# Kernel tuning notes

Measured on AMD Instinct MI355X. Metric: run time of the kernel, lower is better.

## Reference

```python
import jax, jax.numpy as jnp
import numpy as np

N, IN_F, OUT_F, K = 256, 8192, 8320, 16
J = OUT_F - IN_F  # 128


def setup_inputs() -> dict:
    key = jax.random.key(0)
    k1, k2 = jax.random.split(key)
    tensor = jax.random.normal(k1, (N, IN_F), dtype=jnp.float32)
    T = jax.random.normal(k2, (IN_F, J, K), dtype=jnp.float32)
    return {"tensor": tensor, "T": T}


def reference(tensor, T):
    # flatten(start_dim=1) is identity for rank-2 input
    x = tensor.reshape(tensor.shape[0], -1)            # [N, IN_F]
    feats = jnp.einsum('ni,ijk->njk', x, T)            # [N, J, K]
    # pairwise L1 across batch: [N,1,J,K] - [N,J,K] -> [N,N,J,K]
    diff = jnp.abs(feats[:, None, :, :] - feats[None, :, :, :])
    l1 = jnp.sum(diff, axis=3)                         # [N, N, J]
    diversity = jnp.sum(jnp.exp(-l1), axis=1)          # [N, J]
    return jnp.concatenate((x, diversity), axis=1)     # [N, IN_F + J]
```

## Files before the change

### kernel.cpp

```cpp
#include <hip/hip_runtime.h>

typedef unsigned int  u32;
typedef unsigned short u16;

typedef __bf16 bf16x8 __attribute__((ext_vector_type(8)));
typedef float  floatx4 __attribute__((ext_vector_type(4)));

#define N_ROWS 256
#define IN_F   8192
#define OUT_F  8320
#define JDIM   128
#define KDIM   16
#define JK     2048

#define BM     256
#define BN     64
#define BK     64
#define WSTRIDE 72

typedef const __attribute__((address_space(1))) u32 gu32;
typedef __attribute__((address_space(3))) u32 su32;

__device__ __forceinline__ u16 f2bf(float f) {
    u32 u = __float_as_uint(f);
    return (u16)((u + 0x7fffu + ((u >> 16) & 1u)) >> 16);
}
__device__ __forceinline__ float bf2f(u16 h) { return __uint_as_float(((u32)h) << 16); }

__global__ __launch_bounds__(256) void prep_kernel(const float* __restrict__ X,
                                                   float* __restrict__ out,
                                                   u16* __restrict__ Xb)
{
    int t = blockIdx.x * 256 + threadIdx.x;
    float4 v = reinterpret_cast<const float4*>(X)[t];
    int row = t >> 11;
    int c4  = t & 2047;
    reinterpret_cast<float4*>(out + (size_t)row * OUT_F)[c4] = v;
    ushort4 b;
    b.x = f2bf(v.x); b.y = f2bf(v.y); b.z = f2bf(v.z); b.w = f2bf(v.w);
    reinterpret_cast<ushort4*>(Xb)[t] = b;
    if (t < 8192) {
        int r2 = t >> 5, j4 = t & 31;
        reinterpret_cast<float4*>(out + (size_t)r2 * OUT_F + IN_F)[j4] = make_float4(0.f, 0.f, 0.f, 0.f);
    }
}

__global__ __launch_bounds__(256) void gemm_kernel(const u16* __restrict__ Xb,
                                                   const float* __restrict__ W,
                                                   u16* __restrict__ slabs,
                                                   int kchunk)
{
    __shared__ u16 xs[BM * BK];
    __shared__ u16 wt[BN * WSTRIDE];

    const int tid  = threadIdx.x;
    const int lane = tid & 63;
    const int wave = tid >> 6;
    const int c0   = blockIdx.x * BN;
    const int s    = blockIdx.y;
    const int k0base = s * kchunk;

    floatx4 acc[4][4] = {};

    const int xrl = lane >> 3;
    const int xgc = (lane & 7) ^ xrl;
    const int wk  = (tid >> 4) << 2;
    const int wc  = (tid & 15) << 2;

    const float* wptr = W + (size_t)(k0base + wk) * JK + c0 + wc;

    float4 wreg[4];
    #pragma unroll
    for (int r = 0; r < 4; ++r)
        wreg[r] = *(const float4*)(wptr + (size_t)r * JK);

    const int iters = kchunk >> 6;
    for (int it = 0; it < iters; ++it) {
        const int k0 = k0base + it * BK;
        __syncthreads();

        #pragma unroll
        for (int g = 0; g < 8; ++g) {
            int rbase = wave * 64 + g * 8;
            const u16* gp = Xb + (size_t)(rbase + xrl) * IN_F + k0 + xgc * 8;
            u32* lp = (u32*)&xs[rbase * BK];
            __builtin_amdgcn_global_load_lds((gu32*)gp, (su32*)lp, 16, 0, 0);
        }

        {
            const float* wr = (const float*)wreg;
            #pragma unroll
            for (int i = 0; i < 4; ++i) {
                u32 lo = (u32)f2bf(wr[0 * 4 + i]) | ((u32)f2bf(wr[1 * 4 + i]) << 16);
                u32 hi = (u32)f2bf(wr[2 * 4 + i]) | ((u32)f2bf(wr[3 * 4 + i]) << 16);
                uint2 v; v.x = lo; v.y = hi;
                *(uint2*)&wt[(wc + i) * WSTRIDE + wk] = v;
            }
        }
        __syncthreads();

        if (it + 1 < iters) {
            const float* wn = wptr + (size_t)(it + 1) * BK * JK;
            #pragma unroll
            for (int r = 0; r < 4; ++r)
                wreg[r] = *(const float4*)(wn + (size_t)r * JK);
        }

        const int mrow = lane & 15;
        const int q    = lane >> 4;
        #pragma unroll
        for (int h = 0; h < 2; ++h) {
            bf16x8 a[4], b[4];
            #pragma unroll
            for (int rt = 0; rt < 4; ++rt) {
                int rl   = wave * 64 + rt * 16 + mrow;
                int slot = (h * 4 + q) ^ (rl & 7);
                a[rt] = *reinterpret_cast<const bf16x8*>(&xs[rl * BK + slot * 8]);
            }
            #pragma unroll
            for (int ct = 0; ct < 4; ++ct) {
                int col = ct * 16 + mrow;
                b[ct] = *reinterpret_cast<const bf16x8*>(&wt[col * WSTRIDE + (h * 4 + q) * 8]);
            }
            #pragma unroll
            for (int rt = 0; rt < 4; ++rt)
                #pragma unroll
                for (int ct = 0; ct < 4; ++ct)
                    acc[rt][ct] = __builtin_amdgcn_mfma_f32_16x16x32_bf16(a[rt], b[ct], acc[rt][ct], 0, 0, 0);
        }
    }

    const int qe = lane >> 4;
    const int cl = lane & 15;
    u16* sp = slabs + (size_t)s * N_ROWS * JK;
    #pragma unroll
    for (int rt = 0; rt < 4; ++rt)
        #pragma unroll
        for (int ct = 0; ct < 4; ++ct)
            #pragma unroll
            for (int r = 0; r < 4; ++r) {
                int row = wave * 64 + rt * 16 + qe * 4 + r;
                int col = c0 + ct * 16 + cl;
                sp[(size_t)row * JK + col] = f2bf(acc[rt][ct][r]);
            }
}

__global__ __launch_bounds__(256) void reduce_kernel(const u16* __restrict__ slabs,
                                                     float* __restrict__ feats, int S)
{
    int t = blockIdx.x * 256 + threadIdx.x;
    float acc[8] = {};
    for (int s = 0; s < S; ++s) {
        uint4 v = *(const uint4*)(slabs + (size_t)s * N_ROWS * JK + (size_t)t * 8);
        const u16* h = (const u16*)&v;
        #pragma unroll
        for (int e = 0; e < 8; ++e) acc[e] += bf2f(h[e]);
    }
    float4* fp = (float4*)(feats + (size_t)t * 8);
    fp[0] = make_float4(acc[0], acc[1], acc[2], acc[3]);
    fp[1] = make_float4(acc[4], acc[5], acc[6], acc[7]);
}

__global__ __launch_bounds__(256) void pairwise_kernel(const float* __restrict__ feats,
                                                       float* __restrict__ out)
{
    const int j = blockIdx.x;
    const int mq = blockIdx.y;
    const int n = threadIdx.x;

    __shared__ float F[N_ROWS * KDIM];
    const float* fr = feats + (size_t)n * JK + j * KDIM;
    float4 v0 = ((const float4*)fr)[0];
    float4 v1 = ((const float4*)fr)[1];
    float4 v2 = ((const float4*)fr)[2];
    float4 v3 = ((const float4*)fr)[3];
    float4* Fp = (float4*)&F[n * KDIM];
    Fp[0] = v0; Fp[1] = v1; Fp[2] = v2; Fp[3] = v3;
    __syncthreads();

    float f[16] = { v0.x, v0.y, v0.z, v0.w, v1.x, v1.y, v1.z, v1.w,
                    v2.x, v2.y, v2.z, v2.w, v3.x, v3.y, v3.z, v3.w };
    float accum = 0.f;
    const int m0 = mq * 64;
    for (int m = 0; m < 64; ++m) {
        const float* Fm = &F[(m0 + m) * KDIM];
        float l1 = 0.f;
        #pragma unroll
        for (int k = 0; k < 16; ++k) l1 += fabsf(f[k] - Fm[k]);
        accum += exp2f(-1.4426950408889634f * l1);
    }
    atomicAdd(&out[(size_t)n * OUT_F + IN_F + j], accum);
}

extern "C" void kernel_launch(void* const* d_in, const int* in_sizes, int n_in,
                              void* d_out, int out_size, void* d_ws, size_t ws_size,
                              hipStream_t stream)
{
    const float* X = (const float*)d_in[0];
    const float* T = (const float*)d_in[1];
    float* out = (float*)d_out;

    float* feats = (float*)d_ws;
    u16*   Xb    = (u16*)((char*)d_ws + (2u << 20));
    u16*   slabs = (u16*)((char*)d_ws + (6u << 20));

    int S = 16;
    if (ws_size < (6u << 20) + (size_t)16 * N_ROWS * JK * 2) S = 8;
    if (ws_size < (6u << 20) + (size_t)8  * N_ROWS * JK * 2) S = 4;
    int kchunk = IN_F / S;

    prep_kernel<<<2048, 256, 0, stream>>>(X, out, Xb);
    gemm_kernel<<<dim3(JK / BN, S), 256, 0, stream>>>(Xb, T, slabs, kchunk);
    reduce_kernel<<<256, 256, 0, stream>>>(slabs, feats, S);
    pairwise_kernel<<<dim3(JDIM, 4), 256, 0, stream>>>(feats, out);
}
```

Measured before the change: 142.0 us.

## Fuse split-K reduction into pairwise kernel with j-major slab layout

The separate reduce kernel and the fp32 feats buffer are removed. The GEMM now writes its bf16 partial slabs in a j-major layout ([j][row][k]), so each pairwise block can sum the S partial slices for its own j directly while loading features. This saves one kernel launch and a global round trip through feats. In exchange, each of the 4 mq blocks per j re-reads and re-reduces the same slabs, and the GEMM epilogue stores have a different access pattern.

New measurement: 135.5 us. 4.6% less time.

```diff
diff --git a/kernel.cpp b/kernel.cpp
--- a/kernel.cpp
+++ b/kernel.cpp
@@ -17,6 +17,9 @@
 #define BN     64
 #define BK     64
 #define WSTRIDE 72
+
+#define SLAB_U16   (N_ROWS * JK)
+#define JSLICE_U16 (N_ROWS * KDIM)
 
 typedef const __attribute__((address_space(1))) u32 gu32;
 typedef __attribute__((address_space(3))) u32 su32;
@@ -132,56 +135,67 @@
 
     const int qe = lane >> 4;
     const int cl = lane & 15;
-    u16* sp = slabs + (size_t)s * N_ROWS * JK;
+    u16* sp = slabs + (size_t)s * SLAB_U16;
     #pragma unroll
     for (int rt = 0; rt < 4; ++rt)
         #pragma unroll
-        for (int ct = 0; ct < 4; ++ct)
+        for (int ct = 0; ct < 4; ++ct) {
+            int j = (c0 >> 4) + ct;
             #pragma unroll
             for (int r = 0; r < 4; ++r) {
                 int row = wave * 64 + rt * 16 + qe * 4 + r;
-                int col = c0 + ct * 16 + cl;
-                sp[(size_t)row * JK + col] = f2bf(acc[rt][ct][r]);
-            }
-}
-
-__global__ __launch_bounds__(256) void reduce_kernel(const u16* __restrict__ slabs,
-                                                     float* __restrict__ feats, int S)
-{
-    int t = blockIdx.x * 256 + threadIdx.x;
-    float acc[8] = {};
-    for (int s = 0; s < S; ++s) {
-        uint4 v = *(const uint4*)(slabs + (size_t)s * N_ROWS * JK + (size_t)t * 8);
-        const u16* h = (const u16*)&v;
-        #pragma unroll
-        for (int e = 0; e < 8; ++e) acc[e] += bf2f(h[e]);
-    }
-    float4* fp = (float4*)(feats + (size_t)t * 8);
-    fp[0] = make_float4(acc[0], acc[1], acc[2], acc[3]);
-    fp[1] = make_float4(acc[4], acc[5], acc[6], acc[7]);
-}
-
-__global__ __launch_bounds__(256) void pairwise_kernel(const float* __restrict__ feats,
+                sp[(size_t)j * JSLICE_U16 + row * KDIM + cl] = f2bf(acc[rt][ct][r]);
+            }
+        }
+}
+
+template<int S>
+__global__ __launch_bounds__(256) void fused_rp_kernel(const u16* __restrict__ slabs,
                                                        float* __restrict__ out)
 {
-    const int j = blockIdx.x;
+    const int j  = blockIdx.x;
     const int mq = blockIdx.y;
-    const int n = threadIdx.x;
+    const int n  = threadIdx.x;
 
     __shared__ float F[N_ROWS * KDIM];
-    const float* fr = feats + (size_t)n * JK + j * KDIM;
-    float4 v0 = ((const float4*)fr)[0];
-    float4 v1 = ((const float4*)fr)[1];
-    float4 v2 = ((const float4*)fr)[2];
-    float4 v3 = ((const float4*)fr)[3];
+
+    const u16* base = slabs + (size_t)j * JSLICE_U16 + n * KDIM;
+
+    float f[16];
+    #pragma unroll
+    for (int k = 0; k < 16; ++k) f[k] = 0.f;
+
+    #pragma unroll
+    for (int so = 0; so < S; so += 4) {
+        uint4 va[4], vb[4];
+        #pragma unroll
+        for (int i = 0; i < 4; ++i) {
+            const u16* p = base + (size_t)(so + i) * SLAB_U16;
+            va[i] = *(const uint4*)p;
+            vb[i] = *(const uint4*)(p + 8);
+        }
+        #pragma unroll
+        for (int i = 0; i < 4; ++i) {
+            const u16* ha = (const u16*)&va[i];
+            const u16* hb = (const u16*)&vb[i];
+            #pragma unroll
+            for (int e = 0; e < 8; ++e) {
+                f[e]     += bf2f(ha[e]);
+                f[8 + e] += bf2f(hb[e]);
+            }
+        }
+    }
+
     float4* Fp = (float4*)&F[n * KDIM];
-    Fp[0] = v0; Fp[1] = v1; Fp[2] = v2; Fp[3] = v3;
+    Fp[0] = make_float4(f[0],  f[1],  f[2],  f[3]);
+    Fp[1] = make_float4(f[4],  f[5],  f[6],  f[7]);
+    Fp[2] = make_float4(f[8],  f[9],  f[10], f[11]);
+    Fp[3] = make_float4(f[12], f[13], f[14], f[15]);
     __syncthreads();
 
-    float f[16] = { v0.x, v0.y, v0.z, v0.w, v1.x, v1.y, v1.z, v1.w,
-                    v2.x, v2.y, v2.z, v2.w, v3.x, v3.y, v3.z, v3.w };
     float accum = 0.f;
     const int m0 = mq * 64;
+    #pragma unroll 2
     for (int m = 0; m < 64; ++m) {
         const float* Fm = &F[(m0 + m) * KDIM];
         float l1 = 0.f;
@@ -200,17 +214,20 @@
     const float* T = (const float*)d_in[1];
     float* out = (float*)d_out;
 
-    float* feats = (float*)d_ws;
-    u16*   Xb    = (u16*)((char*)d_ws + (2u << 20));
-    u16*   slabs = (u16*)((char*)d_ws + (6u << 20));
+    u16* Xb    = (u16*)d_ws;
+    u16* slabs = (u16*)((char*)d_ws + (4u << 20));
 
     int S = 16;
-    if (ws_size < (6u << 20) + (size_t)16 * N_ROWS * JK * 2) S = 8;
-    if (ws_size < (6u << 20) + (size_t)8  * N_ROWS * JK * 2) S = 4;
+    if (ws_size < (4u << 20) + (size_t)16 * SLAB_U16 * 2) S = 8;
+    if (ws_size < (4u << 20) + (size_t)8  * SLAB_U16 * 2) S = 4;
     int kchunk = IN_F / S;
 
     prep_kernel<<<2048, 256, 0, stream>>>(X, out, Xb);
     gemm_kernel<<<dim3(JK / BN, S), 256, 0, stream>>>(Xb, T, slabs, kchunk);
-    reduce_kernel<<<256, 256, 0, stream>>>(slabs, feats, S);
-    pairwise_kernel<<<dim3(JDIM, 4), 256, 0, stream>>>(feats, out);
-}
+    if (S == 16)
+        fused_rp_kernel<16><<<dim3(JDIM, 4), 256, 0, stream>>>(slabs, out);
+    else if (S == 8)
+        fused_rp_kernel<8><<<dim3(JDIM, 4), 256, 0, stream>>>(slabs, out);
+    else
+        fused_rp_kernel<4><<<dim3(JDIM, 4), 256, 0, stream>>>(slabs, out);
+}
```
